# Kernel tuning notes

Hardware: AMD Instinct MI355X
Metric: run time of the kernel (lower is better)

The kernel has to match this reference:

```python
import jax, jax.numpy as jnp
import numpy as np
from math import pi

N = 256        # in_features == out_features
BATCH = 131072


def givens_orthogonal(angles, n):
    """Build an n x n orthogonal matrix as the ordered product of Givens
    rotations G(i, j, theta_k) over pairs i < j in lexicographic order.
    Each rotation mixes rows i and j; applied sequentially via lax.scan."""
    ii, jj = np.triu_indices(n, 1)  # static pair order, len = n*(n-1)//2
    ii = jnp.asarray(ii, dtype=jnp.int32)
    jj = jnp.asarray(jj, dtype=jnp.int32)

    def body(M, t):
        i, j, th = t
        c, s = jnp.cos(th), jnp.sin(th)
        ri, rj = M[i], M[j]
        M = M.at[i].set(c * ri - s * rj)
        M = M.at[j].set(s * ri + c * rj)
        return M, None

    M0 = jnp.eye(n, dtype=angles.dtype)
    M, _ = jax.lax.scan(body, M0, (ii, jj, angles))
    return M


def setup_inputs() -> dict:
    key = jax.random.key(0)
    k1, k2, k3 = jax.random.split(key, 3)
    n_ang = N * (N - 1) // 2  # 32640
    return {
        "x": jax.random.normal(k1, (BATCH, N), dtype=jnp.float32),
        "Uweight": jax.random.uniform(k2, (n_ang,), minval=-pi / 2, maxval=pi / 2, dtype=jnp.float32),
        "Vweight": jax.random.uniform(k3, (n_ang,), minval=-pi / 2, maxval=pi / 2, dtype=jnp.float32),
        "Sweight": jnp.ones((N,), dtype=jnp.float32),
        "bias": jnp.zeros((N,), dtype=jnp.float32),
    }


def reference(x, Uweight, Vweight, Sweight, bias):
    # W = V @ diag(S) @ U^T  (SVD-parametrized weight, out x in)
    # y = x @ W^T + b = ((x @ U) * S) @ V^T + b   (square case in == out)
    U = givens_orthogonal(Uweight, N)  # (in, in) orthogonal
    V = givens_orthogonal(Vweight, N)  # (out, out) orthogonal
    return ((x @ U) * Sweight) @ V.T + bias
```

## Files before the change

### kernel.cpp

```cpp
#include <hip/hip_runtime.h>
#include <hip/hip_bf16.h>
#include <math.h>

#define NN 256
#define NSEG 32
#define MAT (NN*NN)

#define MATS0 0
#define MATS1 (MATS0 + 64*MAT)
#define WBT_OFF (MATS1 + 32*MAT)

static __device__ const int BD[NSEG+1] =
    {0,4,8,12,16,20,24,28,32,37,42,47,52,57,62,67,73,79,85,91,97,
     104,111,118,126,134,143,153,164,177,192,213,255};
#define CSL_CAP 1120

typedef __attribute__((ext_vector_type(8))) short short8;
typedef __attribute__((ext_vector_type(4))) float f32x4;

__device__ __forceinline__ short f2bf(float f) {
    __hip_bfloat16 h = __float2bfloat16(f);
    return *reinterpret_cast<short*>(&h);
}

#define BAR() do {                                              \
    asm volatile("s_waitcnt lgkmcnt(0)" ::: "memory");          \
    __builtin_amdgcn_s_barrier();                               \
    asm volatile("" ::: "memory");                              \
} while (0)

__global__ __launch_bounds__(64) void k_build(const float* __restrict__ au,
                                              const float* __restrict__ av,
                                              float* __restrict__ mats) {
    int b = blockIdx.x;
    int matid = b >> 7;
    int seg   = (b >> 2) & 31;
    int chunk = b & 3;
    int t = threadIdx.x;
    int c0 = chunk * 64;
    int i0 = BD[seg], i1 = BD[seg+1];
    float* outp = mats + (matid * NSEG + seg) * MAT;

    if (c0 + 64 <= i0) {
        for (int id = t; id < 4096; id += 64) {
            int row = id >> 4, c4 = (id & 15) * 4;
            float4 v = {0.f,0.f,0.f,0.f};
            int d = row - (c0 + c4);
            if (d >= 0 && d < 4) ((float*)&v)[d] = 1.0f;
            *(float4*)(outp + row*NN + c0 + c4) = v;
        }
        return;
    }

    __shared__ float M[NN * 64];
    __shared__ float2 csl[CSL_CAP];

    int kbase = 255*i0 - (i0*(i0-1))/2;
    int kend  = 255*i1 - (i1*(i1-1))/2;
    int nrot  = kend - kbase;
    const float* ang = (matid ? av : au) + kbase;
    for (int idx = t; idx < nrot; idx += 64) {
        float s, c;
        sincosf(ang[idx], &s, &c);
        float2 v = {c, s};
        csl[idx] = v;
    }

    int MR = NN - i0;
    for (int rr = 0; rr < MR; ++rr)
        M[rr*64 + t] = (i0 + rr == c0 + t) ? 1.0f : 0.0f;
    __syncthreads();

    for (int i = i0; i < i1; ++i) {
        int jstart = (i + 1 > c0) ? (i + 1) : c0;
        int kl = 255*i - (i*(i-1))/2 + (jstart - i - 1) - kbase;
        float ri = M[(i - i0)*64 + t];
        int j = jstart;
        int ng = (NN - jstart) >> 3;

        float2 cb[8]; float rj[8];
        if (ng > 0) {
#pragma unroll
            for (int u = 0; u < 8; ++u) cb[u] = csl[kl + u];
#pragma unroll
            for (int u = 0; u < 8; ++u) rj[u] = M[(j - i0 + u)*64 + t];
        }
        for (int g = 0; g < ng; ++g) {
            float2 cn[8]; float rn[8];
            if (g + 1 < ng) {
#pragma unroll
                for (int u = 0; u < 8; ++u) cn[u] = csl[kl + 8 + u];
#pragma unroll
                for (int u = 0; u < 8; ++u) rn[u] = M[(j + 8 - i0 + u)*64 + t];
            }
#pragma unroll
            for (int u = 0; u < 8; ++u) {
                float wv = cb[u].y*ri + cb[u].x*rj[u];
                ri       = cb[u].x*ri - cb[u].y*rj[u];
                M[(j - i0 + u)*64 + t] = wv;
            }
#pragma unroll
            for (int u = 0; u < 8; ++u) { cb[u] = cn[u]; rj[u] = rn[u]; }
            j += 8; kl += 8;
        }
        int rem = NN - j;
        if (rem > 0) {
            float2 cc[7]; float r7[7];
#pragma unroll
            for (int u = 0; u < 7; ++u)
                if (u < rem) { cc[u] = csl[kl + u];
                               r7[u] = M[(j - i0 + u)*64 + t]; }
#pragma unroll
            for (int u = 0; u < 7; ++u)
                if (u < rem) {
                    float wv = cc[u].y*ri + cc[u].x*r7[u];
                    ri       = cc[u].x*ri - cc[u].y*r7[u];
                    M[(j - i0 + u)*64 + t] = wv;
                }
        }
        M[(i - i0)*64 + t] = ri;
    }
    __syncthreads();

    for (int id = t; id < 4096; id += 64) {
        int row = id >> 4, c4 = (id & 15) * 4;
        float4 v;
        if (row < i0) {
            v = make_float4(0.f,0.f,0.f,0.f);
            int d = row - (c0 + c4);
            if (d >= 0 && d < 4) ((float*)&v)[d] = 1.0f;
        } else {
            v = *(const float4*)&M[(row - i0)*64 + c4];
        }
        *(float4*)(outp + row*NN + c0 + c4) = v;
    }
}

__global__ __launch_bounds__(256) void k_fold(const float* __restrict__ in,
                                              float* __restrict__ out,
                                              int nOut, int lg, int span) {
    int b = blockIdx.x;
    int np2 = 2 * nOut;
    int m    = b & (np2 - 1);
    int tile = b >> lg;
    int side = (m >= nOut) ? 1 : 0;
    int q = m - side * nOut;
    const float* A = in + (side*np2 + 2*q + 1) * MAT;
    const float* B = in + (side*np2 + 2*q) * MAT;
    float* C = out + m * MAT;
    int i0A = BD[q * span + (span >> 1)];
    int r0 = (tile >> 2) * 64, c0 = (tile & 3) * 64;
    int t = threadIdx.x;

    if (r0 + 64 <= i0A) {
#pragma unroll
        for (int u = 0; u < 4; ++u) {
            int id = u*256 + t;
            int rr = id >> 4, cc = (id & 15) * 4;
            *(float4*)(C + (r0+rr)*NN + c0 + cc) =
                *(const float4*)(B + (r0+rr)*NN + c0 + cc);
        }
        return;
    }

    int kstart = ((r0 < i0A) ? r0 : i0A) & ~31;
    int nt = (NN - kstart) >> 5;

    __shared__ float Ast[2][32][68];
    __shared__ float Bs [2][32][68];
    int tx = t & 15, ty = t >> 4;
    int arow = t >> 3, ak4 = t & 7;
    int bkr = t >> 4, bc4 = t & 15;

    float acc[4][4] = {};
    f32x4 pa0, pa1, pb0, pb1;
    {
        int kt = kstart;
        pa0 = *(const f32x4*)(A + (r0 + arow     )*NN + kt + ak4*4);
        pa1 = *(const f32x4*)(A + (r0 + arow + 32)*NN + kt + ak4*4);
        pb0 = *(const f32x4*)(B + (kt + bkr      )*NN + c0 + bc4*4);
        pb1 = *(const f32x4*)(B + (kt + bkr + 16 )*NN + c0 + bc4*4);
    }
    for (int it = 0; it < nt; ++it) {
        int cur = it & 1;
#pragma unroll
        for (int jj = 0; jj < 4; ++jj) {
            Ast[cur][ak4*4 + jj][arow]      = pa0[jj];
            Ast[cur][ak4*4 + jj][arow + 32] = pa1[jj];
        }
        *(f32x4*)&Bs[cur][bkr     ][bc4*4] = pb0;
        *(f32x4*)&Bs[cur][bkr + 16][bc4*4] = pb1;
        if (it + 1 < nt) {
            int k2 = kstart + (it+1)*32;
            pa0 = *(const f32x4*)(A + (r0 + arow     )*NN + k2 + ak4*4);
            pa1 = *(const f32x4*)(A + (r0 + arow + 32)*NN + k2 + ak4*4);
            pb0 = *(const f32x4*)(B + (k2 + bkr      )*NN + c0 + bc4*4);
            pb1 = *(const f32x4*)(B + (k2 + bkr + 16 )*NN + c0 + bc4*4);
        }
        BAR();
#pragma unroll 8
        for (int kk = 0; kk < 32; ++kk) {
            f32x4 a4 = *(const f32x4*)&Ast[cur][kk][ty*4];
            f32x4 b4 = *(const f32x4*)&Bs [cur][kk][tx*4];
#pragma unroll
            for (int rr = 0; rr < 4; ++rr)
#pragma unroll
                for (int cc = 0; cc < 4; ++cc)
                    acc[rr][cc] = fmaf(a4[rr], b4[cc], acc[rr][cc]);
        }
    }
#pragma unroll
    for (int rr = 0; rr < 4; ++rr) {
        float4 o = {acc[rr][0], acc[rr][1], acc[rr][2], acc[rr][3]};
        *(float4*)(C + (r0 + ty*4 + rr)*NN + c0 + tx*4) = o;
    }
}

__global__ __launch_bounds__(256) void k_wmatT(const float* __restrict__ U,
                                               const float* __restrict__ V,
                                               const float* __restrict__ S,
                                               unsigned short* __restrict__ Wbt) {
    int b = blockIdx.x;
    int n0 = (b >> 4) * 16, i0 = (b & 15) * 16;
    int t = threadIdx.x, ti = t & 15, tn = t >> 4;
    __shared__ float Us[16][260];
    __shared__ float Vs[16][260];
    {
        int rr = t >> 4, cc = (t & 15) * 16;
#pragma unroll
        for (int q = 0; q < 4; ++q) {
            float4 u = *(const float4*)(U + (i0+rr)*NN + cc + q*4);
            float4 s = *(const float4*)(S + cc + q*4);
            u.x *= s.x; u.y *= s.y; u.z *= s.z; u.w *= s.w;
            *(float4*)&Us[rr][cc+q*4] = u;
            *(float4*)&Vs[rr][cc+q*4] = *(const float4*)(V + (n0+rr)*NN + cc + q*4);
        }
    }
    __syncthreads();
    float acc = 0.f;
#pragma unroll 8
    for (int k4 = 0; k4 < 64; ++k4) {
        float4 uu = *(const float4*)&Us[ti][k4*4];
        float4 vv = *(const float4*)&Vs[tn][k4*4];
        acc += uu.x*vv.x + uu.y*vv.y + uu.z*vv.z + uu.w*vv.w;
    }
    Wbt[(n0+tn)*NN + (i0+ti)] = (unsigned short)f2bf(acc);
}

__global__ __launch_bounds__(512, 4) void k_mm(const float* __restrict__ x,
                                               const unsigned short* __restrict__ Wbt,
                                               const float* __restrict__ bias,
                                               float* __restrict__ out) {
    int t = threadIdx.x;
    int w = t >> 6, l = t & 63, l15 = l & 15, lg = l >> 4;
    int n0 = w * 32;

    __shared__ unsigned short Xs[2][8 * 512];

    long rowbase = (long)blockIdx.x * 256;
    int r = t & 15, m = t >> 4;
    int ksb = m >> 2;
    int lidx = r + 16 * (m & 3);

    const float* s0 = x + (rowbase + r) * NN + 8*m;
    float4 f0 = *(const float4*)(s0);
    float4 f1 = *(const float4*)(s0 + 4);

    short8 bfrag[2][8];
#pragma unroll
    for (int nt = 0; nt < 2; ++nt) {
        const unsigned short* wrow = Wbt + (n0 + nt*16 + l15) * NN + lg * 8;
#pragma unroll
        for (int ks = 0; ks < 8; ++ks)
            bfrag[nt][ks] = *(const short8*)(wrow + ks * 32);
    }
    float b0 = bias[n0 + l15];
    float b1 = bias[n0 + 16 + l15];

    for (int it = 0; it < 16; ++it) {
        int cur = it & 1;
        short8 h;
        h[0]=f2bf(f0.x); h[1]=f2bf(f0.y); h[2]=f2bf(f0.z); h[3]=f2bf(f0.w);
        h[4]=f2bf(f1.x); h[5]=f2bf(f1.y); h[6]=f2bf(f1.z); h[7]=f2bf(f1.w);
        *(short8*)&Xs[cur][ksb*512 + lidx*8] = h;
        if (it < 15) {
            const float* sn = x + (rowbase + (it+1)*16 + r) * NN + 8*m;
            f0 = *(const float4*)(sn);
            f1 = *(const float4*)(sn + 4);
        }
        BAR();

        f32x4 acc0 = {0.f,0.f,0.f,0.f}, acc1 = {0.f,0.f,0.f,0.f};
#pragma unroll
        for (int ks = 0; ks < 8; ++ks) {
            short8 af = *(const short8*)&Xs[cur][ks*512 + l*8];
            acc0 = __builtin_amdgcn_mfma_f32_16x16x32_bf16(af, bfrag[0][ks], acc0, 0, 0, 0);
            acc1 = __builtin_amdgcn_mfma_f32_16x16x32_bf16(af, bfrag[1][ks], acc1, 0, 0, 0);
        }
        float* op = out + (rowbase + it*16 + lg*4) * NN + n0 + l15;
#pragma unroll
        for (int rr = 0; rr < 4; ++rr) {
            op[rr * NN]      = acc0[rr] + b0;
            op[rr * NN + 16] = acc1[rr] + b1;
        }
    }
}

extern "C" void kernel_launch(void* const* d_in, const int* in_sizes, int n_in,
                              void* d_out, int out_size, void* d_ws, size_t ws_size,
                              hipStream_t stream) {
    const float* x    = (const float*)d_in[0];
    const float* Uw   = (const float*)d_in[1];
    const float* Vw   = (const float*)d_in[2];
    const float* Sw   = (const float*)d_in[3];
    const float* bias = (const float*)d_in[4];
    float* out = (float*)d_out;
    float* ws  = (float*)d_ws;

    k_build<<<256, 64, 0, stream>>>(Uw, Vw, ws + MATS0);
    k_fold<<<16*32, 256, 0, stream>>>(ws + MATS0, ws + MATS1, 16, 5, 2);
    k_fold<<<16*16, 256, 0, stream>>>(ws + MATS1, ws + MATS0,  8, 4, 4);
    k_fold<<<16* 8, 256, 0, stream>>>(ws + MATS0, ws + MATS1,  4, 3, 8);
    k_fold<<<16* 4, 256, 0, stream>>>(ws + MATS1, ws + MATS0,  2, 2, 16);
    k_fold<<<16* 2, 256, 0, stream>>>(ws + MATS0, ws + MATS1,  1, 1, 32);
    k_wmatT<<<256, 256, 0, stream>>>(ws + MATS1, ws + MATS1 + MAT, Sw,
                                     (unsigned short*)(ws + WBT_OFF));
    k_mm<<<512, 512, 0, stream>>>(x, (unsigned short*)(ws + WBT_OFF), bias, out);
}
```

Measured before the change: 195.3 us.

## Stage GEMM output through LDS for coalesced stores, halve rows per block, specialize folds

The main GEMM kernel now writes each 16x256 output tile into shared memory and then stores it with per-thread contiguous float4 writes, replacing scattered 4-byte column stores. Each block now handles 128 rows instead of 256, doubling the grid to 1024 blocks. The fold kernels are split into five specialized entry points with compile-time parameters. This adds an extra barrier and 16KB of LDS per block, which may limit occupancy, and loads the B fragments twice as often in total.

After: 200.8 us. 2.8% more time.

```diff
diff --git a/kernel.cpp b/kernel.cpp
--- a/kernel.cpp
+++ b/kernel.cpp
@@ -136,10 +136,10 @@
     }
 }
 
-__global__ __launch_bounds__(256) void k_fold(const float* __restrict__ in,
-                                              float* __restrict__ out,
-                                              int nOut, int lg, int span) {
-    int b = blockIdx.x;
+__device__ __forceinline__ void fold_body(const float* __restrict__ in,
+                                          float* __restrict__ out,
+                                          int nOut, int lg, int span,
+                                          int b, int t) {
     int np2 = 2 * nOut;
     int m    = b & (np2 - 1);
     int tile = b >> lg;
@@ -150,7 +150,6 @@
     float* C = out + m * MAT;
     int i0A = BD[q * span + (span >> 1)];
     int r0 = (tile >> 2) * 64, c0 = (tile & 3) * 64;
-    int t = threadIdx.x;
 
     if (r0 + 64 <= i0A) {
 #pragma unroll
@@ -215,6 +214,17 @@
         *(float4*)(C + (r0 + ty*4 + rr)*NN + c0 + tx*4) = o;
     }
 }
+
+__global__ __launch_bounds__(256) void k_fold1(const float* in, float* out)
+{ fold_body(in, out, 16, 5,  2, blockIdx.x, threadIdx.x); }
+__global__ __launch_bounds__(256) void k_fold2(const float* in, float* out)
+{ fold_body(in, out,  8, 4,  4, blockIdx.x, threadIdx.x); }
+__global__ __launch_bounds__(256) void k_fold3(const float* in, float* out)
+{ fold_body(in, out,  4, 3,  8, blockIdx.x, threadIdx.x); }
+__global__ __launch_bounds__(256) void k_fold4(const float* in, float* out)
+{ fold_body(in, out,  2, 2, 16, blockIdx.x, threadIdx.x); }
+__global__ __launch_bounds__(256) void k_fold5(const float* in, float* out)
+{ fold_body(in, out,  1, 1, 32, blockIdx.x, threadIdx.x); }
 
 __global__ __launch_bounds__(256) void k_wmatT(const float* __restrict__ U,
                                                const float* __restrict__ V,
@@ -256,11 +266,14 @@
     int n0 = w * 32;
 
     __shared__ unsigned short Xs[2][8 * 512];
-
-    long rowbase = (long)blockIdx.x * 256;
+    __shared__ float Os[16 * 256];
+
+    long rowbase = (long)blockIdx.x * 128;
     int r = t & 15, m = t >> 4;
     int ksb = m >> 2;
     int lidx = r + 16 * (m & 3);
+    int ro = t >> 5;
+    int c8 = (t & 31) * 8;
 
     const float* s0 = x + (rowbase + r) * NN + 8*m;
     float4 f0 = *(const float4*)(s0);
@@ -274,16 +287,16 @@
         for (int ks = 0; ks < 8; ++ks)
             bfrag[nt][ks] = *(const short8*)(wrow + ks * 32);
     }
-    float b0 = bias[n0 + l15];
-    float b1 = bias[n0 + 16 + l15];
-
-    for (int it = 0; it < 16; ++it) {
+    float4 bb0 = *(const float4*)(bias + c8);
+    float4 bb1 = *(const float4*)(bias + c8 + 4);
+
+    for (int it = 0; it < 8; ++it) {
         int cur = it & 1;
         short8 h;
         h[0]=f2bf(f0.x); h[1]=f2bf(f0.y); h[2]=f2bf(f0.z); h[3]=f2bf(f0.w);
         h[4]=f2bf(f1.x); h[5]=f2bf(f1.y); h[6]=f2bf(f1.z); h[7]=f2bf(f1.w);
         *(short8*)&Xs[cur][ksb*512 + lidx*8] = h;
-        if (it < 15) {
+        if (it < 7) {
             const float* sn = x + (rowbase + (it+1)*16 + r) * NN + 8*m;
             f0 = *(const float4*)(sn);
             f1 = *(const float4*)(sn + 4);
@@ -297,12 +310,20 @@
             acc0 = __builtin_amdgcn_mfma_f32_16x16x32_bf16(af, bfrag[0][ks], acc0, 0, 0, 0);
             acc1 = __builtin_amdgcn_mfma_f32_16x16x32_bf16(af, bfrag[1][ks], acc1, 0, 0, 0);
         }
-        float* op = out + (rowbase + it*16 + lg*4) * NN + n0 + l15;
 #pragma unroll
         for (int rr = 0; rr < 4; ++rr) {
-            op[rr * NN]      = acc0[rr] + b0;
-            op[rr * NN + 16] = acc1[rr] + b1;
-        }
+            Os[(lg*4 + rr)*256 + n0 + l15]      = acc0[rr];
+            Os[(lg*4 + rr)*256 + n0 + 16 + l15] = acc1[rr];
+        }
+        BAR();
+
+        f32x4 v0 = *(const f32x4*)&Os[ro*256 + c8];
+        f32x4 v1 = *(const f32x4*)&Os[ro*256 + c8 + 4];
+        float4 o0 = {v0[0]+bb0.x, v0[1]+bb0.y, v0[2]+bb0.z, v0[3]+bb0.w};
+        float4 o1 = {v1[0]+bb1.x, v1[1]+bb1.y, v1[2]+bb1.z, v1[3]+bb1.w};
+        float* op = out + (rowbase + it*16 + ro) * NN + c8;
+        *(float4*)(op)     = o0;
+        *(float4*)(op + 4) = o1;
     }
 }
 
@@ -318,12 +339,12 @@
     float* ws  = (float*)d_ws;
 
     k_build<<<256, 64, 0, stream>>>(Uw, Vw, ws + MATS0);
-    k_fold<<<16*32, 256, 0, stream>>>(ws + MATS0, ws + MATS1, 16, 5, 2);
-    k_fold<<<16*16, 256, 0, stream>>>(ws + MATS1, ws + MATS0,  8, 4, 4);
-    k_fold<<<16* 8, 256, 0, stream>>>(ws + MATS0, ws + MATS1,  4, 3, 8);
-    k_fold<<<16* 4, 256, 0, stream>>>(ws + MATS1, ws + MATS0,  2, 2, 16);
-    k_fold<<<16* 2, 256, 0, stream>>>(ws + MATS0, ws + MATS1,  1, 1, 32);
+    k_fold1<<<16*32, 256, 0, stream>>>(ws + MATS0, ws + MATS1);
+    k_fold2<<<16*16, 256, 0, stream>>>(ws + MATS1, ws + MATS0);
+    k_fold3<<<16* 8, 256, 0, stream>>>(ws + MATS0, ws + MATS1);
+    k_fold4<<<16* 4, 256, 0, stream>>>(ws + MATS1, ws + MATS0);
+    k_fold5<<<16* 2, 256, 0, stream>>>(ws + MATS0, ws + MATS1);
     k_wmatT<<<256, 256, 0, stream>>>(ws + MATS1, ws + MATS1 + MAT, Sw,
                                      (unsigned short*)(ws + WBT_OFF));
-    k_mm<<<512, 512, 0, stream>>>(x, (unsigned short*)(ws + WBT_OFF), bias, out);
-}
+    k_mm<<<1024, 512, 0, stream>>>(x, (unsigned short*)(ws + WBT_OFF), bias, out);
+}
```
